# Kernel tuning notes

Hardware: AMD Instinct MI355X
Metric: run time of the kernel (lower is better)

## Reference

```python
import jax, jax.numpy as jnp
import numpy as np

DIM, DEPTH, HEADS, FF = 768, 4, 12, 3072
B, T = 2, 2048
DK = DIM // HEADS
EPS = 1e-5


def _pos_encoding(T, D):
    pos = jnp.arange(T, dtype=jnp.float32)[:, None]                      # [T,1]
    div = jnp.exp(jnp.arange(0, D, 2, dtype=jnp.float32) * (-np.log(10000.0) / D))
    pe = jnp.zeros((T, D), dtype=jnp.float32)
    pe = pe.at[:, 0::2].set(jnp.sin(pos * div))
    pe = pe.at[:, 1::2].set(jnp.cos(pos * div))
    return pe


def _layernorm(x, g, b):
    mu = jnp.mean(x, axis=-1, keepdims=True)
    var = jnp.mean(jnp.square(x - mu), axis=-1, keepdims=True)
    return (x - mu) * jax.lax.rsqrt(var + EPS) * g + b


def setup_inputs() -> dict:
    key = jax.random.key(0)
    ks = jax.random.split(key, 8)
    s = 0.02
    x = jax.random.normal(ks[0], (B, T, DIM), dtype=jnp.float32)
    mask = jnp.tril(jnp.ones((T, T), dtype=jnp.int32))[None, None]        # causal [1,1,T,T]
    return {
        "x": x,
        "mask": mask,
        "qkv_w": jax.random.normal(ks[1], (DEPTH, DIM, 3 * DIM)) * s,
        "qkv_b": jnp.zeros((DEPTH, 3 * DIM)),
        "out_w": jax.random.normal(ks[2], (DEPTH, DIM, DIM)) * s,
        "out_b": jnp.zeros((DEPTH, DIM)),
        "ff1_w": jax.random.normal(ks[3], (DEPTH, DIM, FF)) * s,
        "ff1_b": jnp.zeros((DEPTH, FF)),
        "ff2_w": jax.random.normal(ks[4], (DEPTH, FF, DIM)) * s,
        "ff2_b": jnp.zeros((DEPTH, DIM)),
        "ln1_g": jnp.ones((DEPTH, DIM)),
        "ln1_b": jnp.zeros((DEPTH, DIM)),
        "ln2_g": jnp.ones((DEPTH, DIM)),
        "ln2_b": jnp.zeros((DEPTH, DIM)),
    }


def reference(x, mask, qkv_w, qkv_b, out_w, out_b, ff1_w, ff1_b, ff2_w, ff2_b,
              ln1_g, ln1_b, ln2_g, ln2_b):
    Bx, Tx, D = x.shape
    x = x + _pos_encoding(Tx, D)[None]
    neg = jnp.asarray(-jnp.inf, x.dtype)

    def block(h, p):
        (qw, qb, ow, ob, f1w, f1b, f2w, f2b, g1, b1, g2, b2) = p
        qkv = (h @ qw + qb).reshape(Bx, Tx, 3, HEADS, DK)
        q, k, v = [jnp.transpose(qkv[:, :, i], (0, 2, 1, 3)) for i in range(3)]  # [B,H,T,dk]
        scores = jnp.einsum('bhtd,bhsd->bhts', q, k) / (DK ** 0.5)
        scores = jnp.where(mask == 0, neg, scores)
        attn = jax.nn.softmax(scores, axis=-1)
        ctx = jnp.einsum('bhts,bhsd->bhtd', attn, v)
        ctx = jnp.transpose(ctx, (0, 2, 1, 3)).reshape(Bx, Tx, D)
        h = _layernorm(h + ctx @ ow + ob, g1, b1)
        ff = jnp.maximum(h @ f1w + f1b, 0.0) @ f2w + f2b
        h = _layernorm(h + ff, g2, b2)
        return h, None

    params = (qkv_w, qkv_b, out_w, out_b, ff1_w, ff1_b, ff2_w, ff2_b,
              ln1_g, ln1_b, ln2_g, ln2_b)
    x, _ = jax.lax.scan(block, x, params)
    return x
```

## Files before the change

### kernel.cpp

```cpp
#include <hip/hip_runtime.h>
#include <hip/hip_bf16.h>
#include <math.h>

#define DIMX 768
#define DEPTH 4
#define NHEADS 12
#define FFDIM 3072
#define BBATCH 2
#define TSEQ 2048
#define DKH 64
#define MROWS (BBATCH * TSEQ)
#define NBH (BBATCH * NHEADS)

typedef __attribute__((ext_vector_type(8))) short short8;
typedef __attribute__((ext_vector_type(4))) float f32x4;
typedef __attribute__((ext_vector_type(2))) unsigned uint2v;

__device__ __forceinline__ short f2bf(float f) {
    union { float f; unsigned u; } v; v.f = f;
    unsigned r = v.u + 0x7fff + ((v.u >> 16) & 1);
    return (short)(r >> 16);
}
__device__ __forceinline__ unsigned pack2bf(float a, float b) {
    return ((unsigned)(unsigned short)f2bf(b) << 16) | (unsigned short)f2bf(a);
}

__global__ __launch_bounds__(256) void pe_add_kernel(const float* __restrict__ x,
                                                     float* __restrict__ h,
                                                     short* __restrict__ hb) {
    int idx = blockIdx.x * 256 + threadIdx.x;
    int total = MROWS * DIMX;
    if (idx >= total) return;
    int d = idx % DIMX;
    int t = (idx / DIMX) % TSEQ;
    int i2 = d & ~1;
    float div = expf((float)i2 * (-9.210340371976184f / (float)DIMX));
    float ang = (float)t * div;
    float pe = (d & 1) ? cosf(ang) : sinf(ang);
    float r = x[idx] + pe;
    h[idx] = r;
    hb[idx] = f2bf(r);
}

__global__ __launch_bounds__(256) void wt_kernel(const float* __restrict__ in,
                                                 short* __restrict__ out,
                                                 int K, int N) {
    __shared__ float t[32][33];
    const int tid = threadIdx.x;
    const int c = tid & 31;
    const int r = tid >> 5;
    const int n0 = blockIdx.x * 32;
    const int k0 = blockIdx.y * 32;
#pragma unroll
    for (int i = 0; i < 4; i++)
        t[r + 8 * i][c] = in[(size_t)(k0 + r + 8 * i) * N + n0 + c];
    __syncthreads();
#pragma unroll
    for (int i = 0; i < 4; i++)
        out[(size_t)(n0 + r + 8 * i) * K + k0 + c] = f2bf(t[c][r + 8 * i]);
}

template <int RELU, int BF16OUT>
__global__ __launch_bounds__(256) void gemm_bf16_kernel(
    const short* __restrict__ A,
    const short* __restrict__ BT,
    const float* __restrict__ bias,
    float* __restrict__ Cf,
    short* __restrict__ Cb,
    int M, int N, int K) {
    __shared__ __align__(16) short As[128 * 32];
    __shared__ __align__(16) short Bs[128 * 32];

    const int tid = threadIdx.x;
    const int lane = tid & 63;
    const int w = tid >> 6;
    const int wm = w >> 1, wn = w & 1;
    const int r0 = blockIdx.y * 128;
    const int c0 = blockIdx.x * 128;

    f32x4 acc[4][4];
#pragma unroll
    for (int i = 0; i < 4; i++)
#pragma unroll
        for (int j = 0; j < 4; j++) acc[i][j] = f32x4{0.f, 0.f, 0.f, 0.f};

    const int srow = lane >> 2;
    const int skel = (lane & 3) * 8;
    const short* Ag0 = A + (size_t)(r0 + w * 16 + srow) * K + skel;
    const short* Ag1 = A + (size_t)(r0 + (4 + w) * 16 + srow) * K + skel;
    const short* Bg0 = BT + (size_t)(c0 + w * 16 + srow) * K + skel;
    const short* Bg1 = BT + (size_t)(c0 + (4 + w) * 16 + srow) * K + skel;

    char* AsB = (char*)As;
    char* BsB = (char*)Bs;

    for (int k0 = 0; k0 < K; k0 += 32) {
        __syncthreads();
        __builtin_amdgcn_global_load_lds(
            (const __attribute__((address_space(1))) void*)(Ag0 + k0),
            (__attribute__((address_space(3))) void*)(AsB + (size_t)w * 1024), 16, 0, 0);
        __builtin_amdgcn_global_load_lds(
            (const __attribute__((address_space(1))) void*)(Ag1 + k0),
            (__attribute__((address_space(3))) void*)(AsB + (size_t)(4 + w) * 1024), 16, 0, 0);
        __builtin_amdgcn_global_load_lds(
            (const __attribute__((address_space(1))) void*)(Bg0 + k0),
            (__attribute__((address_space(3))) void*)(BsB + (size_t)w * 1024), 16, 0, 0);
        __builtin_amdgcn_global_load_lds(
            (const __attribute__((address_space(1))) void*)(Bg1 + k0),
            (__attribute__((address_space(3))) void*)(BsB + (size_t)(4 + w) * 1024), 16, 0, 0);
        __syncthreads();

        short8 af[4], bfr[4];
#pragma unroll
        for (int i = 0; i < 4; i++) {
            af[i]  = *(const short8*)&As[(wm * 64 + i * 16 + (lane & 15)) * 32 + (lane >> 4) * 8];
            bfr[i] = *(const short8*)&Bs[(wn * 64 + i * 16 + (lane & 15)) * 32 + (lane >> 4) * 8];
        }
#pragma unroll
        for (int mi = 0; mi < 4; mi++)
#pragma unroll
            for (int ni = 0; ni < 4; ni++)
                acc[mi][ni] = __builtin_amdgcn_mfma_f32_16x16x32_bf16(
                    af[mi], bfr[ni], acc[mi][ni], 0, 0, 0);
    }

#pragma unroll
    for (int mi = 0; mi < 4; mi++) {
#pragma unroll
        for (int ni = 0; ni < 4; ni++) {
            const int col = c0 + wn * 64 + ni * 16 + (lane & 15);
            const float bv = bias[col];
#pragma unroll
            for (int i = 0; i < 4; i++) {
                const int row = r0 + wm * 64 + mi * 16 + (lane >> 4) * 4 + i;
                float v = acc[mi][ni][i] + bv;
                if (RELU) v = fmaxf(v, 0.f);
                if (BF16OUT) Cb[(size_t)row * N + col] = f2bf(v);
                else         Cf[(size_t)row * N + col] = v;
            }
        }
    }
}

__global__ __launch_bounds__(256) void vt_kernel(const short* __restrict__ qkvb,
                                                 short* __restrict__ vt) {
    __shared__ short tile[64][72];
    const int tid = threadIdx.x;
    const int bh = blockIdx.x % NBH;
    const int s0 = (blockIdx.x / NBH) * 64;
    const int b = bh / NHEADS, h = bh % NHEADS;
    const int r = tid >> 3, c8 = (tid & 7) * 8;
#pragma unroll
    for (int i = 0; i < 2; ++i) {
        const int s = r + 32 * i;
        short8 v = *(const short8*)(qkvb + ((size_t)b * TSEQ + s0 + s) * (3 * DIMX)
                                    + 2 * DIMX + h * DKH + c8);
#pragma unroll
        for (int e = 0; e < 8; ++e) tile[c8 + e][s] = v[e];
    }
    __syncthreads();
#pragma unroll
    for (int i = 0; i < 2; ++i) {
        const int d = r + 32 * i;
        short8 o = *(const short8*)&tile[d][c8];
        *(short8*)(vt + ((size_t)bh * DKH + d) * TSEQ + s0 + c8) = o;
    }
}

__device__ __forceinline__ void attn_process_qb(
    f32x4* SF, f32x4* OF, float& m, float& l,
    const short* Vs, int s0, int trow, bool maskq, int g, int q) {
    float mx = -3.0e38f;
#pragma unroll
    for (int f = 0; f < 4; ++f) {
#pragma unroll
        for (int i = 0; i < 4; ++i) {
            float v = SF[f][i] * 0.125f;
            if (maskq && (s0 + 16 * f + 4 * g + i > trow)) v = -1e30f;
            SF[f][i] = v;
            mx = fmaxf(mx, v);
        }
    }
    mx = fmaxf(mx, __shfl_xor(mx, 16));
    mx = fmaxf(mx, __shfl_xor(mx, 32));
    const float mnew = fmaxf(m, mx);
    const float corr = __expf(m - mnew);
    float ts = 0.f;
    unsigned pk01[4], pk23[4];
#pragma unroll
    for (int f = 0; f < 4; ++f) {
#pragma unroll
        for (int i = 0; i < 4; ++i) {
            float p = __expf(SF[f][i] - mnew);
            SF[f][i] = p;
            ts += p;
        }
        pk01[f] = pack2bf(SF[f][0], SF[f][1]);
        pk23[f] = pack2bf(SF[f][2], SF[f][3]);
    }
    ts += __shfl_xor(ts, 16);
    ts += __shfl_xor(ts, 32);
    l = l * corr + ts;
    m = mnew;
#pragma unroll
    for (int d = 0; d < 4; ++d) OF[d] *= corr;

    const int lsrc = ((g & 1) << 5) + q;
    const bool fhi = (g >> 1) != 0;
#pragma unroll
    for (int kb = 0; kb < 2; ++kb) {
        unsigned w0a = __shfl((int)pk01[2 * kb],     lsrc);
        unsigned w1a = __shfl((int)pk23[2 * kb],     lsrc);
        unsigned w0b = __shfl((int)pk01[2 * kb + 1], lsrc);
        unsigned w1b = __shfl((int)pk23[2 * kb + 1], lsrc);
        unsigned w2a = __shfl((int)pk01[2 * kb],     lsrc + 16);
        unsigned w3a = __shfl((int)pk23[2 * kb],     lsrc + 16);
        unsigned w2b = __shfl((int)pk01[2 * kb + 1], lsrc + 16);
        unsigned w3b = __shfl((int)pk23[2 * kb + 1], lsrc + 16);
        union { unsigned u[4]; short8 v; } bb;
        bb.u[0] = fhi ? w0b : w0a;
        bb.u[1] = fhi ? w1b : w1a;
        bb.u[2] = fhi ? w2b : w2a;
        bb.u[3] = fhi ? w3b : w3a;
#pragma unroll
        for (int db = 0; db < 4; ++db) {
            const int row = 16 * db + q;
            short8 vf = *(const short8*)&Vs[row * 64 + ((((kb << 2) + g)) ^ (q & 7)) * 8];
            OF[db] = __builtin_amdgcn_mfma_f32_16x16x32_bf16(vf, bb.v, OF[db], 0, 0, 0);
        }
    }
}

__global__ __launch_bounds__(256) void attn_mfma_kernel(
    const short* __restrict__ qkvb, const short* __restrict__ vt,
    short* __restrict__ ctx) {
    __shared__ __align__(16) short Ks[64 * 64];
    __shared__ __align__(16) short Vs[64 * 64];

    const int tid = threadIdx.x;
    const int lane = tid & 63;
    const int w = tid >> 6;
    const int g = lane >> 4;
    const int q = lane & 15;

    const int bh = blockIdx.x % NBH;
    const int j  = 15 - blockIdx.x / NBH;
    const int b = bh / NHEADS, h = bh % NHEADS;
    const int q0 = j * 128;
    const int base0 = q0 + w * 16;
    const int base1 = q0 + 64 + w * 16;
    const int trow0 = base0 + q;
    const int trow1 = base1 + q;

    short8 QF[2][2];
    {
        const short* qp0 = qkvb + ((size_t)b * TSEQ + trow0) * (3 * DIMX) + h * DKH;
        const short* qp1 = qkvb + ((size_t)b * TSEQ + trow1) * (3 * DIMX) + h * DKH;
        QF[0][0] = *(const short8*)(qp0 + g * 8);
        QF[0][1] = *(const short8*)(qp0 + 32 + g * 8);
        QF[1][0] = *(const short8*)(qp1 + g * 8);
        QF[1][1] = *(const short8*)(qp1 + 32 + g * 8);
    }

    f32x4 OF0[4], OF1[4];
#pragma unroll
    for (int d = 0; d < 4; ++d) {
        OF0[d] = f32x4{0.f, 0.f, 0.f, 0.f};
        OF1[d] = f32x4{0.f, 0.f, 0.f, 0.f};
    }
    float m0 = -INFINITY, l0 = 0.f, m1 = -INFINITY, l1 = 0.f;

    const int srow = lane >> 3;
    const int slot = lane & 7;
    const int sw8 = ((slot ^ srow)) * 8;

    const short* kcol = qkvb + (size_t)b * TSEQ * (3 * DIMX) + DIMX + h * DKH;
    const short* vrow = vt + (size_t)bh * DKH * TSEQ;

    const int ntiles = 2 * j + 2;
    for (int tix = 0; tix < ntiles; ++tix) {
        const int s0 = tix * 64;
        const bool do0 = (tix != ntiles - 1);
        __syncthreads();
#pragma unroll
        for (int iss = 0; iss < 2; ++iss) {
            const int rb = 8 * w + 32 * iss;
            const short* ksrc = kcol + (size_t)(s0 + rb + srow) * (3 * DIMX) + sw8;
            const short* vsrc = vrow + (size_t)(rb + srow) * TSEQ + s0 + sw8;
            __builtin_amdgcn_global_load_lds(
                (const __attribute__((address_space(1))) void*)ksrc,
                (__attribute__((address_space(3))) void*)((char*)Ks + rb * 128), 16, 0, 0);
            __builtin_amdgcn_global_load_lds(
                (const __attribute__((address_space(1))) void*)vsrc,
                (__attribute__((address_space(3))) void*)((char*)Vs + rb * 128), 16, 0, 0);
        }
        __syncthreads();

        f32x4 SF0[4], SF1[4];
#pragma unroll
        for (int f = 0; f < 4; ++f) {
            SF0[f] = f32x4{0.f, 0.f, 0.f, 0.f};
            SF1[f] = f32x4{0.f, 0.f, 0.f, 0.f};
        }
#pragma unroll
        for (int f = 0; f < 4; ++f) {
            const int rx = (16 * f + q) * 64;
            const int r7 = q & 7;
#pragma unroll
            for (int kd = 0; kd < 2; ++kd) {
                short8 kf = *(const short8*)&Ks[rx + (((kd << 2) + g) ^ r7) * 8];
                if (do0)
                    SF0[f] = __builtin_amdgcn_mfma_f32_16x16x32_bf16(kf, QF[0][kd], SF0[f], 0, 0, 0);
                SF1[f] = __builtin_amdgcn_mfma_f32_16x16x32_bf16(kf, QF[1][kd], SF1[f], 0, 0, 0);
            }
        }

        if (do0) {
            const bool mq0 = (s0 + 63 > base0);
            attn_process_qb(SF0, OF0, m0, l0, Vs, s0, trow0, mq0, g, q);
        }
        const bool mq1 = (s0 + 63 > base1);
        attn_process_qb(SF1, OF1, m1, l1, Vs, s0, trow1, mq1, g, q);
    }

    const float inv0 = 1.f / l0;
    const float inv1 = 1.f / l1;
#pragma unroll
    for (int db = 0; db < 4; ++db) {
        uint2v o0, o1;
        o0.x = pack2bf(OF0[db][0] * inv0, OF0[db][1] * inv0);
        o0.y = pack2bf(OF0[db][2] * inv0, OF0[db][3] * inv0);
        o1.x = pack2bf(OF1[db][0] * inv1, OF1[db][1] * inv1);
        o1.y = pack2bf(OF1[db][2] * inv1, OF1[db][3] * inv1);
        *(uint2v*)(ctx + ((size_t)b * TSEQ + trow0) * DIMX + h * DKH + db * 16 + g * 4) = o0;
        *(uint2v*)(ctx + ((size_t)b * TSEQ + trow1) * DIMX + h * DKH + db * 16 + g * 4) = o1;
    }
}

__global__ __launch_bounds__(256) void ln_kernel(const float* __restrict__ resid,
                                                 const float* __restrict__ y,
                                                 const float* __restrict__ g,
                                                 const float* __restrict__ bta,
                                                 float* __restrict__ out,
                                                 short* __restrict__ outb) {
    const int row = blockIdx.x;
    const int tid = threadIdx.x;
    __shared__ float red[4];

    float v[3];
#pragma unroll
    for (int i = 0; i < 3; i++) {
        int idx = tid + i * 256;
        size_t p = (size_t)row * DIMX + idx;
        v[i] = resid[p] + y[p];
    }
    float part = v[0] + v[1] + v[2];
#pragma unroll
    for (int off = 32; off; off >>= 1) part += __shfl_xor(part, off, 64);
    if ((tid & 63) == 0) red[tid >> 6] = part;
    __syncthreads();
    const float mean = (red[0] + red[1] + red[2] + red[3]) * (1.f / 768.f);

    float p2 = 0.f;
#pragma unroll
    for (int i = 0; i < 3; i++) {
        float d = v[i] - mean;
        p2 += d * d;
    }
#pragma unroll
    for (int off = 32; off; off >>= 1) p2 += __shfl_xor(p2, off, 64);
    __syncthreads();
    if ((tid & 63) == 0) red[tid >> 6] = p2;
    __syncthreads();
    const float var = (red[0] + red[1] + red[2] + red[3]) * (1.f / 768.f);
    const float inv = rsqrtf(var + 1e-5f);

#pragma unroll
    for (int i = 0; i < 3; i++) {
        int idx = tid + i * 256;
        float r = (v[i] - mean) * inv * g[idx] + bta[idx];
        out[(size_t)row * DIMX + idx] = r;
        outb[(size_t)row * DIMX + idx] = f2bf(r);
    }
}

extern "C" void kernel_launch(void* const* d_in, const int* in_sizes, int n_in,
                              void* d_out, int out_size, void* d_ws, size_t ws_size,
                              hipStream_t stream) {
    (void)in_sizes; (void)n_in; (void)out_size; (void)ws_size;
    const float* x     = (const float*)d_in[0];
    const float* qkv_w = (const float*)d_in[2];
    const float* qkv_b = (const float*)d_in[3];
    const float* out_w = (const float*)d_in[4];
    const float* out_b = (const float*)d_in[5];
    const float* ff1_w = (const float*)d_in[6];
    const float* ff1_b = (const float*)d_in[7];
    const float* ff2_w = (const float*)d_in[8];
    const float* ff2_b = (const float*)d_in[9];
    const float* ln1_g = (const float*)d_in[10];
    const float* ln1_b = (const float*)d_in[11];
    const float* ln2_g = (const float*)d_in[12];
    const float* ln2_b = (const float*)d_in[13];

    char* p = (char*)d_ws;
    float* h      = (float*)p;  p += (size_t)MROWS * DIMX * 4;
    float* y      = (float*)p;  p += (size_t)MROWS * DIMX * 4;
    short* h_bf   = (short*)p;  p += (size_t)MROWS * DIMX * 2;
    short* ctx_bf = (short*)p;  p += (size_t)MROWS * DIMX * 2;
    short* ff_bf  = (short*)p;  p += (size_t)MROWS * FFDIM * 2;
    short* qkv_bf = (short*)p;  p += (size_t)MROWS * 3 * DIMX * 2;
    short* vtb    = (short*)p;  p += (size_t)NBH * DKH * TSEQ * 2;
    short* qkvT   = (short*)p;  p += (size_t)DEPTH * 3 * DIMX * DIMX * 2;
    short* outT   = (short*)p;  p += (size_t)DEPTH * DIMX * DIMX * 2;
    short* ff1T   = (short*)p;  p += (size_t)DEPTH * FFDIM * DIMX * 2;
    short* ff2T   = (short*)p;  p += (size_t)DEPTH * DIMX * FFDIM * 2;

    for (int l = 0; l < DEPTH; ++l) {
        wt_kernel<<<dim3(3 * DIMX / 32, DIMX / 32), 256, 0, stream>>>(
            qkv_w + (size_t)l * DIMX * 3 * DIMX, qkvT + (size_t)l * 3 * DIMX * DIMX,
            DIMX, 3 * DIMX);
        wt_kernel<<<dim3(DIMX / 32, DIMX / 32), 256, 0, stream>>>(
            out_w + (size_t)l * DIMX * DIMX, outT + (size_t)l * DIMX * DIMX,
            DIMX, DIMX);
        wt_kernel<<<dim3(FFDIM / 32, DIMX / 32), 256, 0, stream>>>(
            ff1_w + (size_t)l * DIMX * FFDIM, ff1T + (size_t)l * FFDIM * DIMX,
            DIMX, FFDIM);
        wt_kernel<<<dim3(DIMX / 32, FFDIM / 32), 256, 0, stream>>>(
            ff2_w + (size_t)l * FFDIM * DIMX, ff2T + (size_t)l * DIMX * FFDIM,
            FFDIM, DIMX);
    }

    pe_add_kernel<<<(MROWS * DIMX + 255) / 256, 256, 0, stream>>>(x, h, h_bf);

    for (int l = 0; l < DEPTH; ++l) {
        gemm_bf16_kernel<0, 1><<<dim3(3 * DIMX / 128, MROWS / 128), 256, 0, stream>>>(
            h_bf, qkvT + (size_t)l * 3 * DIMX * DIMX, qkv_b + (size_t)l * 3 * DIMX,
            nullptr, qkv_bf, MROWS, 3 * DIMX, DIMX);
        vt_kernel<<<NBH * (TSEQ / 64), 256, 0, stream>>>(qkv_bf, vtb);
        attn_mfma_kernel<<<NBH * 16, 256, 0, stream>>>(qkv_bf, vtb, ctx_bf);
        gemm_bf16_kernel<0, 0><<<dim3(DIMX / 128, MROWS / 128), 256, 0, stream>>>(
            ctx_bf, outT + (size_t)l * DIMX * DIMX, out_b + (size_t)l * DIMX,
            y, nullptr, MROWS, DIMX, DIMX);
        ln_kernel<<<MROWS, 256, 0, stream>>>(h, y, ln1_g + (size_t)l * DIMX,
                                             ln1_b + (size_t)l * DIMX, h, h_bf);
        gemm_bf16_kernel<1, 1><<<dim3(FFDIM / 128, MROWS / 128), 256, 0, stream>>>(
            h_bf, ff1T + (size_t)l * FFDIM * DIMX, ff1_b + (size_t)l * FFDIM,
            nullptr, ff_bf, MROWS, FFDIM, DIMX);
        gemm_bf16_kernel<0, 0><<<dim3(DIMX / 128, MROWS / 128), 256, 0, stream>>>(
            ff_bf, ff2T + (size_t)l * DIMX * FFDIM, ff2_b + (size_t)l * DIMX,
            y, nullptr, MROWS, DIMX, FFDIM);
        ln_kernel<<<MROWS, 256, 0, stream>>>(h, y, ln2_g + (size_t)l * DIMX,
                                             ln2_b + (size_t)l * DIMX, h, h_bf);
    }
    hipMemcpyAsync(d_out, h, (size_t)MROWS * DIMX * sizeof(float),
                   hipMemcpyDeviceToDevice, stream);
}
```

Baseline: 1.292 ms.

## Double-buffer K/V tiles in attention, shrink query block, lazy rescale

The attention kernel now uses two LDS buffers so the next K/V tile's global-to-LDS load is issued while the current tile is computed. This replaces the two barriers per tile with one waitcnt plus barrier. Each block now handles 64 query rows instead of 128, doubling the grid to 768 blocks for better occupancy and load balance. The online softmax only rescales when the running max rises by more than 8, skipping the correction multiply most of the time, and s_setprio is raised around the MFMA sections. In exchange the kernel uses more LDS, and each K/V tile is loaded by twice as many blocks overall.

```diff
diff --git a/kernel.cpp b/kernel.cpp
--- a/kernel.cpp
+++ b/kernel.cpp
@@ -183,15 +183,20 @@
     }
     mx = fmaxf(mx, __shfl_xor(mx, 16));
     mx = fmaxf(mx, __shfl_xor(mx, 32));
-    const float mnew = fmaxf(m, mx);
-    const float corr = __expf(m - mnew);
+    if (mx > m + 8.f) {
+        const float corr = __expf(m - mx);
+#pragma unroll
+        for (int d = 0; d < 4; ++d) OF[d] *= corr;
+        l *= corr;
+        m = mx;
+    }
     float ts = 0.f;
     unsigned pk01[4], pk23[4];
 #pragma unroll
     for (int f = 0; f < 4; ++f) {
 #pragma unroll
         for (int i = 0; i < 4; ++i) {
-            float p = __expf(SF[f][i] - mnew);
+            float p = __expf(SF[f][i] - m);
             SF[f][i] = p;
             ts += p;
         }
@@ -200,13 +205,11 @@
     }
     ts += __shfl_xor(ts, 16);
     ts += __shfl_xor(ts, 32);
-    l = l * corr + ts;
-    m = mnew;
-#pragma unroll
-    for (int d = 0; d < 4; ++d) OF[d] *= corr;
+    l += ts;
 
     const int lsrc = ((g & 1) << 5) + q;
     const bool fhi = (g >> 1) != 0;
+    __builtin_amdgcn_s_setprio(1);
 #pragma unroll
     for (int kb = 0; kb < 2; ++kb) {
         unsigned w0a = __shfl((int)pk01[2 * kb],     lsrc);
@@ -229,13 +232,14 @@
             OF[db] = __builtin_amdgcn_mfma_f32_16x16x32_bf16(vf, bb.v, OF[db], 0, 0, 0);
         }
     }
+    __builtin_amdgcn_s_setprio(0);
 }
 
 __global__ __launch_bounds__(256) void attn_mfma_kernel(
     const short* __restrict__ qkvb, const short* __restrict__ vt,
     short* __restrict__ ctx) {
-    __shared__ __align__(16) short Ks[64 * 64];
-    __shared__ __align__(16) short Vs[64 * 64];
+    __shared__ __align__(16) short Ks[2][64 * 64];
+    __shared__ __align__(16) short Vs[2][64 * 64];
 
     const int tid = threadIdx.x;
     const int lane = tid & 63;
@@ -244,96 +248,91 @@
     const int q = lane & 15;
 
     const int bh = blockIdx.x % NBH;
-    const int j  = 15 - blockIdx.x / NBH;
+    const int j  = 31 - blockIdx.x / NBH;
     const int b = bh / NHEADS, h = bh % NHEADS;
-    const int q0 = j * 128;
-    const int base0 = q0 + w * 16;
-    const int base1 = q0 + 64 + w * 16;
-    const int trow0 = base0 + q;
-    const int trow1 = base1 + q;
-
-    short8 QF[2][2];
+    const int q0 = j * 64;
+    const int base = q0 + w * 16;
+    const int trow = base + q;
+
+    short8 QF[2];
     {
-        const short* qp0 = qkvb + ((size_t)b * TSEQ + trow0) * (3 * DIMX) + h * DKH;
-        const short* qp1 = qkvb + ((size_t)b * TSEQ + trow1) * (3 * DIMX) + h * DKH;
-        QF[0][0] = *(const short8*)(qp0 + g * 8);
-        QF[0][1] = *(const short8*)(qp0 + 32 + g * 8);
-        QF[1][0] = *(const short8*)(qp1 + g * 8);
-        QF[1][1] = *(const short8*)(qp1 + 32 + g * 8);
-    }
-
-    f32x4 OF0[4], OF1[4];
-#pragma unroll
-    for (int d = 0; d < 4; ++d) {
-        OF0[d] = f32x4{0.f, 0.f, 0.f, 0.f};
-        OF1[d] = f32x4{0.f, 0.f, 0.f, 0.f};
-    }
-    float m0 = -INFINITY, l0 = 0.f, m1 = -INFINITY, l1 = 0.f;
+        const short* qp = qkvb + ((size_t)b * TSEQ + trow) * (3 * DIMX) + h * DKH;
+        QF[0] = *(const short8*)(qp + g * 8);
+        QF[1] = *(const short8*)(qp + 32 + g * 8);
+    }
+
+    f32x4 OF[4];
+#pragma unroll
+    for (int d = 0; d < 4; ++d) OF[d] = f32x4{0.f, 0.f, 0.f, 0.f};
+    float m = -INFINITY, l = 0.f;
 
     const int srow = lane >> 3;
     const int slot = lane & 7;
-    const int sw8 = ((slot ^ srow)) * 8;
+    const int sw8 = (slot ^ srow) * 8;
 
     const short* kcol = qkvb + (size_t)b * TSEQ * (3 * DIMX) + DIMX + h * DKH;
     const short* vrow = vt + (size_t)bh * DKH * TSEQ;
 
-    const int ntiles = 2 * j + 2;
+    const int ntiles = j + 1;
+
+#define STAGE(BUF, TIX)                                                        \
+    {                                                                          \
+        const int s0_ = (TIX) * 64;                                            \
+        _Pragma("unroll")                                                      \
+        for (int iss = 0; iss < 2; ++iss) {                                    \
+            const int rb = 8 * w + 32 * iss;                                   \
+            const short* ksrc = kcol + (size_t)(s0_ + rb + srow) * (3 * DIMX) + sw8; \
+            const short* vsrc = vrow + (size_t)(rb + srow) * TSEQ + s0_ + sw8; \
+            __builtin_amdgcn_global_load_lds(                                  \
+                (const __attribute__((address_space(1))) void*)ksrc,           \
+                (__attribute__((address_space(3))) void*)((char*)&Ks[BUF][0] + rb * 128), 16, 0, 0); \
+            __builtin_amdgcn_global_load_lds(                                  \
+                (const __attribute__((address_space(1))) void*)vsrc,           \
+                (__attribute__((address_space(3))) void*)((char*)&Vs[BUF][0] + rb * 128), 16, 0, 0); \
+        }                                                                      \
+    }
+
+    STAGE(0, 0)
+    asm volatile("s_waitcnt vmcnt(0)" ::: "memory");
+    __builtin_amdgcn_s_barrier();
+
     for (int tix = 0; tix < ntiles; ++tix) {
+        const int cur = tix & 1;
+        if (tix + 1 < ntiles) STAGE(cur ^ 1, tix + 1)
         const int s0 = tix * 64;
-        const bool do0 = (tix != ntiles - 1);
-        __syncthreads();
-#pragma unroll
-        for (int iss = 0; iss < 2; ++iss) {
-            const int rb = 8 * w + 32 * iss;
-            const short* ksrc = kcol + (size_t)(s0 + rb + srow) * (3 * DIMX) + sw8;
-            const short* vsrc = vrow + (size_t)(rb + srow) * TSEQ + s0 + sw8;
-            __builtin_amdgcn_global_load_lds(
-                (const __attribute__((address_space(1))) void*)ksrc,
-                (__attribute__((address_space(3))) void*)((char*)Ks + rb * 128), 16, 0, 0);
-            __builtin_amdgcn_global_load_lds(
-                (const __attribute__((address_space(1))) void*)vsrc,
-                (__attribute__((address_space(3))) void*)((char*)Vs + rb * 128), 16, 0, 0);
-        }
-        __syncthreads();
-
-        f32x4 SF0[4], SF1[4];
-#pragma unroll
-        for (int f = 0; f < 4; ++f) {
-            SF0[f] = f32x4{0.f, 0.f, 0.f, 0.f};
-            SF1[f] = f32x4{0.f, 0.f, 0.f, 0.f};
-        }
+        const short* Kb = &Ks[cur][0];
+        const short* Vb = &Vs[cur][0];
+
+        f32x4 SF[4];
+#pragma unroll
+        for (int f = 0; f < 4; ++f) SF[f] = f32x4{0.f, 0.f, 0.f, 0.f};
+        __builtin_amdgcn_s_setprio(1);
 #pragma unroll
         for (int f = 0; f < 4; ++f) {
             const int rx = (16 * f + q) * 64;
             const int r7 = q & 7;
 #pragma unroll
             for (int kd = 0; kd < 2; ++kd) {
-                short8 kf = *(const short8*)&Ks[rx + (((kd << 2) + g) ^ r7) * 8];
-                if (do0)
-                    SF0[f] = __builtin_amdgcn_mfma_f32_16x16x32_bf16(kf, QF[0][kd], SF0[f], 0, 0, 0);
-                SF1[f] = __builtin_amdgcn_mfma_f32_16x16x32_bf16(kf, QF[1][kd], SF1[f], 0, 0, 0);
+                short8 kf = *(const short8*)&Kb[rx + (((kd << 2) + g) ^ r7) * 8];
+                SF[f] = __builtin_amdgcn_mfma_f32_16x16x32_bf16(kf, QF[kd], SF[f], 0, 0, 0);
             }
         }
-
-        if (do0) {
-            const bool mq0 = (s0 + 63 > base0);
-            attn_process_qb(SF0, OF0, m0, l0, Vs, s0, trow0, mq0, g, q);
-        }
-        const bool mq1 = (s0 + 63 > base1);
-        attn_process_qb(SF1, OF1, m1, l1, Vs, s0, trow1, mq1, g, q);
-    }
-
-    const float inv0 = 1.f / l0;
-    const float inv1 = 1.f / l1;
+        __builtin_amdgcn_s_setprio(0);
+
+        attn_process_qb(SF, OF, m, l, Vb, s0, trow, tix == ntiles - 1, g, q);
+
+        asm volatile("s_waitcnt vmcnt(0)" ::: "memory");
+        __builtin_amdgcn_s_barrier();
+    }
+#undef STAGE
+
+    const float inv = 1.f / l;
 #pragma unroll
     for (int db = 0; db < 4; ++db) {
-        uint2v o0, o1;
-        o0.x = pack2bf(OF0[db][0] * inv0, OF0[db][1] * inv0);
-        o0.y = pack2bf(OF0[db][2] * inv0, OF0[db][3] * inv0);
-        o1.x = pack2bf(OF1[db][0] * inv1, OF1[db][1] * inv1);
-        o1.y = pack2bf(OF1[db][2] * inv1, OF1[db][3] * inv1);
-        *(uint2v*)(ctx + ((size_t)b * TSEQ + trow0) * DIMX + h * DKH + db * 16 + g * 4) = o0;
-        *(uint2v*)(ctx + ((size_t)b * TSEQ + trow1) * DIMX + h * DKH + db * 16 + g * 4) = o1;
+        uint2v o;
+        o.x = pack2bf(OF[db][0] * inv, OF[db][1] * inv);
+        o.y = pack2bf(OF[db][2] * inv, OF[db][3] * inv);
+        *(uint2v*)(ctx + ((size_t)b * TSEQ + trow) * DIMX + h * DKH + db * 16 + g * 4) = o;
     }
 }
 
@@ -437,7 +436,7 @@
             h_bf, qkvT + (size_t)l * 3 * DIMX * DIMX, qkv_b + (size_t)l * 3 * DIMX,
             nullptr, qkv_bf, MROWS, 3 * DIMX, DIMX);
         vt_kernel<<<NBH * (TSEQ / 64), 256, 0, stream>>>(qkv_bf, vtb);
-        attn_mfma_kernel<<<NBH * 16, 256, 0, stream>>>(qkv_bf, vtb, ctx_bf);
+        attn_mfma_kernel<<<NBH * 32, 256, 0, stream>>>(qkv_bf, vtb, ctx_bf);
         gemm_bf16_kernel<0, 0><<<dim3(DIMX / 128, MROWS / 128), 256, 0, stream>>>(
             ctx_bf, outT + (size_t)l * DIMX * DIMX, out_b + (size_t)l * DIMX,
             y, nullptr, MROWS, DIMX, DIMX);
```

Measured after the change: 1.118 ms. 13.5% less time.
